# Kernel optimization log

Measured on AMD Instinct MI355X. Metric: run time of the kernel, lower is better.

## Reference

```python
import jax, jax.numpy as jnp
import numpy as np


def setup_inputs() -> dict:
    key = jax.random.key(0)
    k1, k2 = jax.random.split(key)
    node_num = 10000
    n_edges = 640000
    d = 128
    embs = jax.random.normal(k1, (node_num, d), dtype=jnp.float32)
    ratings = jax.random.randint(k2, (n_edges, 2), 0, node_num, dtype=jnp.int32)
    return {"embs": embs, "ratings": ratings, "node_num": node_num}


def reference(embs, ratings, node_num):
    # edge endpoints: row (source) and column (neighbor) indices
    r0 = ratings[:, 0]
    r1 = ratings[:, 1]
    # edge dot-product attention scores  [E]
    scores = jnp.sum(embs[r0] * embs[r1], axis=-1)
    # sparse row-wise softmax (torch.sparse.softmax over dim=1)
    seg_max = jax.ops.segment_max(scores, r0, num_segments=node_num)
    seg_max = jnp.where(jnp.isfinite(seg_max), seg_max, jnp.float32(0.0))  # empty rows
    ex = jnp.exp(scores - seg_max[r0])
    denom = jax.ops.segment_sum(ex, r0, num_segments=node_num)
    attn = ex / denom[r0]
    # attention weights are detached in the original module
    attn = jax.lax.stop_gradient(attn)
    # sparse mm aggregation: out[i] = sum_{e: r0[e]=i} attn[e] * embs[r1[e]]
    out = jax.ops.segment_sum(attn[:, None] * embs[r1], r0, num_segments=node_num)
    return out
```

## Files before the change

### kernel.cpp

```cpp
#include <hip/hip_runtime.h>
#include <hip/hip_bf16.h>
#include <hip/hip_fp16.h>
#include <math.h>


#define K_CHUNKS 256
#define NODE_LDS 10240
#define NPAD 10240
#define STAGE_LDS 2560
#define EXP_CLAMP 80.0f
#define MAXE_N 256

using half2v = _Float16 __attribute__((ext_vector_type(2)));

__device__ __forceinline__ half2v u2h(unsigned int x) {
    return __builtin_bit_cast(half2v, x);
}

__global__ __launch_bounds__(1024) void build_kernel(const int2* __restrict__ ratings,
                             unsigned short* __restrict__ mtmp,
                             unsigned short* __restrict__ staging,
                             const float4* __restrict__ embs4,
                             ushort4* __restrict__ embs16,
                             int n_edges, int node_num, int chunk_size) {
    __shared__ int hist[NODE_LDS];
    __shared__ unsigned short stage[STAGE_LDS];
    __shared__ int lds_ws[16];
    __shared__ int lds_wp[16];

    int tid  = threadIdx.x;
    int lane = tid & 63;
    int wid  = tid >> 6;
    int k    = blockIdx.x;

    for (int i = tid; i < NODE_LDS; i += 1024) hist[i] = 0;
    __syncthreads();

    int base = k * chunk_size;
    int end  = base + chunk_size; if (end > n_edges) end = n_edges;

    int e0i = base + tid, e1i = e0i + 1024, e2i = e1i + 1024;
    bool h0 = e0i < end, h1 = e1i < end, h2 = e2i < end;
    int2 r0v = h0 ? ratings[e0i] : make_int2(0, 0);
    int2 r1v = h1 ? ratings[e1i] : make_int2(0, 0);
    int2 r2v = h2 ? ratings[e2i] : make_int2(0, 0);

    {
        int nf4 = node_num * 32;
        int per = (nf4 + (int)gridDim.x - 1) / (int)gridDim.x;
        int s0 = k * per;
        int s1 = s0 + per; if (s1 > nf4) s1 = nf4;
        for (int i = s0 + tid; i < s1; i += 1024) {
            float4 v = embs4[i];
            __half hx = __float2half(v.x), hy = __float2half(v.y);
            __half hz = __float2half(v.z), hw = __float2half(v.w);
            ushort4 o;
            o.x = *reinterpret_cast<unsigned short*>(&hx);
            o.y = *reinterpret_cast<unsigned short*>(&hy);
            o.z = *reinterpret_cast<unsigned short*>(&hz);
            o.w = *reinterpret_cast<unsigned short*>(&hw);
            embs16[i] = o;
        }
    }

    if (h0) atomicAdd(&hist[r0v.x], 1);
    if (h1) atomicAdd(&hist[r1v.x], 1);
    if (h2) atomicAdd(&hist[r2v.x], 1);
    for (int e = base + 3072 + tid; e < end; e += 1024)
        atomicAdd(&hist[ratings[e].x], 1);
    __syncthreads();

    const int B = NODE_LDS / 1024;
    int b0 = tid * B;
    int c[B];
    int local = 0;
    #pragma unroll
    for (int j = 0; j < B; ++j) {
        c[j] = hist[b0 + j];
        local += c[j];
    }
    int incl = local;
    #pragma unroll
    for (int off = 1; off < 64; off <<= 1) {
        int t = __shfl_up(incl, off, 64);
        if (lane >= off) incl += t;
    }
    if (lane == 63) lds_ws[wid] = incl;
    __syncthreads();
    if (wid == 0 && lane < 16) {
        int wv = lds_ws[lane];
        #pragma unroll
        for (int off = 1; off < 16; off <<= 1) {
            int t = __shfl_up(wv, off, 64);
            if (lane >= off) wv += t;
        }
        lds_wp[lane] = wv;
    }
    __syncthreads();
    int run = ((wid > 0) ? lds_wp[wid - 1] : 0) + (incl - local);

    unsigned int mpack[B / 2];
    #pragma unroll
    for (int j = 0; j < B; ++j) {
        int i = b0 + j;
        int cc = (c[j] > 15) ? 15 : c[j];
        unsigned int m = (((unsigned int)run << 4) | (unsigned int)cc) & 0xffffu;
        if (j & 1) mpack[j >> 1] |= m << 16;
        else       mpack[j >> 1]  = m;
        hist[i] = run;
        run += c[j];
    }
    {
        unsigned int* mrow2 = (unsigned int*)(mtmp + (size_t)k * NPAD) + tid * (B / 2);
        #pragma unroll
        for (int jj = 0; jj < B / 2; ++jj) mrow2[jj] = mpack[jj];
    }
    __syncthreads();

    if (h0) { int p = atomicAdd(&hist[r0v.x], 1); if (p < STAGE_LDS) stage[p] = (unsigned short)r0v.y; }
    if (h1) { int p = atomicAdd(&hist[r1v.x], 1); if (p < STAGE_LDS) stage[p] = (unsigned short)r1v.y; }
    if (h2) { int p = atomicAdd(&hist[r2v.x], 1); if (p < STAGE_LDS) stage[p] = (unsigned short)r2v.y; }
    for (int e = base + 3072 + tid; e < end; e += 1024) {
        int2 r = ratings[e];
        int p = atomicAdd(&hist[r.x], 1);
        if (p < STAGE_LDS) stage[p] = (unsigned short)r.y;
    }
    __syncthreads();

    int nsh = end - base;
    unsigned int* g  = (unsigned int*)(staging + (size_t)k * chunk_size);
    unsigned int* sg = (unsigned int*)stage;
    int nu = (nsh + 1) >> 1;
    for (int i = tid; i < nu; i += 1024) g[i] = sg[i];
}

__global__ __launch_bounds__(256, 8) void node_kernel(
                            const unsigned short* __restrict__ embs16,
                            const unsigned short* __restrict__ mtmp,
                            const unsigned short* __restrict__ staging,
                            float* __restrict__ out,
                            int node_num, int chunk_size) {
    __shared__ int s_r1[4][MAXE_N];

    int tid   = threadIdx.x;
    int lane  = tid & 63;
    int wid   = tid >> 6;
    int g     = lane >> 4;
    int t     = lane & 15;
    int n     = blockIdx.x * 4 + wid;
    bool nvalid = (n < node_num);
    int nc    = nvalid ? n : 0;

    uint4 au = ((const uint4*)(embs16 + (size_t)nc * 128))[t];

    unsigned int f[4];
    #pragma unroll
    for (int j = 0; j < 4; ++j)
        f[j] = mtmp[(size_t)(4 * lane + j) * NPAD + nc];
    int c[4], o[4];
    #pragma unroll
    for (int j = 0; j < 4; ++j) {
        c[j] = nvalid ? (int)(f[j] & 15u) : 0;
        o[j] = (int)(f[j] >> 4);
    }
    int cnt = (c[0] + c[1]) + (c[2] + c[3]);
    int incl = cnt;
    #pragma unroll
    for (int off = 1; off < 64; off <<= 1) {
        int tt = __shfl_up(incl, off, 64);
        if (lane >= off) incl += tt;
    }
    int basep = incl - cnt;
    int E = __shfl(incl, 63, 64);
    if (E > MAXE_N) E = MAXE_N;

    {
        int idx = basep;
        #pragma unroll
        for (int j = 0; j < 4; ++j) {
            if (c[j] > 0) {
                const unsigned short* sp =
                    staging + (size_t)(4 * lane + j) * chunk_size + o[j];
                for (int q = 0; q < c[j]; ++q) {
                    if (idx < MAXE_N) s_r1[wid][idx] = (int)sp[q];
                    ++idx;
                }
            }
        }
    }

    float l = 0.f;
    float acc[8];
    #pragma unroll
    for (int j = 0; j < 8; ++j) acc[j] = 0.f;

    int r1c[4];
    #pragma unroll
    for (int b = 0; b < 4; ++b) {
        int ix = b * 4 + g;
        r1c[b] = (ix < E) ? s_r1[wid][ix] : 0;
    }

    for (int base = 0; base < E; base += 16) {
        uint4 uc[4];
        #pragma unroll
        for (int b = 0; b < 4; ++b)
            uc[b] = ((const uint4*)(embs16 + (size_t)r1c[b] * 128))[t];

        int r1n[4];
        #pragma unroll
        for (int b = 0; b < 4; ++b) {
            int ix = base + 16 + b * 4 + g;
            r1n[b] = (ix < E) ? s_r1[wid][ix] : 0;
        }

        float s[4];
        #pragma unroll
        for (int b = 0; b < 4; ++b) {
            float d = __builtin_amdgcn_fdot2(u2h(uc[b].x), u2h(au.x), 0.f, false);
            d = __builtin_amdgcn_fdot2(u2h(uc[b].y), u2h(au.y), d, false);
            d = __builtin_amdgcn_fdot2(u2h(uc[b].z), u2h(au.z), d, false);
            d = __builtin_amdgcn_fdot2(u2h(uc[b].w), u2h(au.w), d, false);
            s[b] = d;
        }
        #pragma unroll
        for (int b = 0; b < 4; ++b) {
            #pragma unroll
            for (int off = 1; off < 16; off <<= 1)
                s[b] += __shfl_xor(s[b], off, 64);
        }
        float p[4];
        #pragma unroll
        for (int b = 0; b < 4; ++b)
            p[b] = ((base + b * 4 + g) < E) ? __expf(fminf(s[b], EXP_CLAMP)) : 0.f;
        l += (p[0] + p[1]) + (p[2] + p[3]);

        #pragma unroll
        for (int b = 0; b < 4; ++b) {
            half2v h0 = u2h(uc[b].x), h1 = u2h(uc[b].y);
            half2v h2 = u2h(uc[b].z), h3 = u2h(uc[b].w);
            acc[0] = fmaf(p[b], (float)h0[0], acc[0]);
            acc[1] = fmaf(p[b], (float)h0[1], acc[1]);
            acc[2] = fmaf(p[b], (float)h1[0], acc[2]);
            acc[3] = fmaf(p[b], (float)h1[1], acc[3]);
            acc[4] = fmaf(p[b], (float)h2[0], acc[4]);
            acc[5] = fmaf(p[b], (float)h2[1], acc[5]);
            acc[6] = fmaf(p[b], (float)h3[0], acc[6]);
            acc[7] = fmaf(p[b], (float)h3[1], acc[7]);
        }

        #pragma unroll
        for (int b = 0; b < 4; ++b) r1c[b] = r1n[b];
    }

    #pragma unroll
    for (int off = 16; off <= 32; off <<= 1) {
        l += __shfl_xor(l, off, 64);
        #pragma unroll
        for (int j = 0; j < 8; ++j) acc[j] += __shfl_xor(acc[j], off, 64);
    }

    if (g == 0 && nvalid) {
        float inv = (l > 0.f) ? 1.f / l : 0.f;
        float4* orow = (float4*)(out + (size_t)n * 128);
        orow[2 * t]     = make_float4(acc[0] * inv, acc[1] * inv, acc[2] * inv, acc[3] * inv);
        orow[2 * t + 1] = make_float4(acc[4] * inv, acc[5] * inv, acc[6] * inv, acc[7] * inv);
    }
}

extern "C" void kernel_launch(void* const* d_in, const int* in_sizes, int n_in,
                              void* d_out, int out_size, void* d_ws, size_t ws_size,
                              hipStream_t stream) {
    const float* embs    = (const float*)d_in[0];
    const int*   ratings = (const int*)d_in[1];
    const int d        = 128;
    const int node_num = in_sizes[0] / d;
    const int n_edges  = in_sizes[1] / 2;
    float* out = (float*)d_out;

    int chunk_size = (n_edges + K_CHUNKS - 1) / K_CHUNKS;
    if (chunk_size & 1) chunk_size += 1;

    auto align256 = [](size_t x) { return (x + 255) & ~(size_t)255; };
    char* ws = (char*)d_ws;
    unsigned short* mtmp = (unsigned short*)ws;
    ws += align256((size_t)K_CHUNKS * NPAD * 2);
    unsigned short* staging = (unsigned short*)ws;
    ws += align256((size_t)K_CHUNKS * chunk_size * 2 + 32);
    unsigned short* embs16 = (unsigned short*)ws;
    ws += align256((size_t)node_num * 128 * 2);

    build_kernel<<<K_CHUNKS, 1024, 0, stream>>>(
        (const int2*)ratings, mtmp, staging,
        (const float4*)embs, (ushort4*)embs16, n_edges, node_num, chunk_size);

    {
        int blocks = (node_num + 3) / 4;
        node_kernel<<<blocks, 256, 0, stream>>>(
            embs16, mtmp, staging, out, node_num, chunk_size);
    }
}
```

Before: 114.8 us.

## Replace per-chunk LDS bucketing with global-atomic CSR build and pipelined gathers

Replaces the single chunked build kernel, which kept per-chunk histograms and packed 4-bit counts, with a global pipeline: zero counters, a global-atomic histogram fused with the fp16 conversion, a single-block scan, and an atomic scatter into a true CSR. The node kernel then reads row_ptr and copies neighbours directly, removing the 256-way per-chunk lookup and its prefix scan, and it now prefetches the next batch's embedding rows instead of only their indices. This trades one kernel for five launches and moves the edge atomics from LDS to global memory, where they contend more. The per-node edge cap rises to 512.

```diff
diff --git a/kernel.cpp b/kernel.cpp
--- a/kernel.cpp
+++ b/kernel.cpp
@@ -4,12 +4,9 @@
 #include <math.h>
 
 
-#define K_CHUNKS 256
-#define NODE_LDS 10240
-#define NPAD 10240
-#define STAGE_LDS 2560
+#define NODE_PAD 10240
+#define MAXE_N 512
 #define EXP_CLAMP 80.0f
-#define MAXE_N 256
 
 using half2v = _Float16 __attribute__((ext_vector_type(2)));
 
@@ -17,129 +14,92 @@
     return __builtin_bit_cast(half2v, x);
 }
 
-__global__ __launch_bounds__(1024) void build_kernel(const int2* __restrict__ ratings,
-                             unsigned short* __restrict__ mtmp,
-                             unsigned short* __restrict__ staging,
-                             const float4* __restrict__ embs4,
-                             ushort4* __restrict__ embs16,
-                             int n_edges, int node_num, int chunk_size) {
-    __shared__ int hist[NODE_LDS];
-    __shared__ unsigned short stage[STAGE_LDS];
-    __shared__ int lds_ws[16];
-    __shared__ int lds_wp[16];
-
+__global__ __launch_bounds__(1024) void zero_kernel(unsigned int* __restrict__ gcount) {
+    gcount[blockIdx.x * 1024 + threadIdx.x] = 0u;
+}
+
+__global__ __launch_bounds__(256) void hist_conv_kernel(
+        const int2* __restrict__ ratings, unsigned int* __restrict__ gcount,
+        const float4* __restrict__ embs4, ushort4* __restrict__ embs16,
+        int n_edges, int nf4) {
+    int gid    = blockIdx.x * 256 + threadIdx.x;
+    int stride = gridDim.x * 256;
+    for (int e = gid; e < n_edges; e += stride)
+        atomicAdd(&gcount[ratings[e].x], 1u);
+    for (int i = gid; i < nf4; i += stride) {
+        float4 v = embs4[i];
+        __half hx = __float2half(v.x), hy = __float2half(v.y);
+        __half hz = __float2half(v.z), hw = __float2half(v.w);
+        ushort4 o;
+        o.x = *reinterpret_cast<unsigned short*>(&hx);
+        o.y = *reinterpret_cast<unsigned short*>(&hy);
+        o.z = *reinterpret_cast<unsigned short*>(&hz);
+        o.w = *reinterpret_cast<unsigned short*>(&hw);
+        embs16[i] = o;
+    }
+}
+
+__global__ __launch_bounds__(1024) void scan_kernel(
+        const unsigned int* __restrict__ gcount,
+        unsigned int* __restrict__ row_ptr,
+        unsigned int* __restrict__ cursor) {
+    __shared__ unsigned int lds_ws[16];
+    __shared__ unsigned int lds_wp[16];
     int tid  = threadIdx.x;
     int lane = tid & 63;
     int wid  = tid >> 6;
-    int k    = blockIdx.x;
-
-    for (int i = tid; i < NODE_LDS; i += 1024) hist[i] = 0;
-    __syncthreads();
-
-    int base = k * chunk_size;
-    int end  = base + chunk_size; if (end > n_edges) end = n_edges;
-
-    int e0i = base + tid, e1i = e0i + 1024, e2i = e1i + 1024;
-    bool h0 = e0i < end, h1 = e1i < end, h2 = e2i < end;
-    int2 r0v = h0 ? ratings[e0i] : make_int2(0, 0);
-    int2 r1v = h1 ? ratings[e1i] : make_int2(0, 0);
-    int2 r2v = h2 ? ratings[e2i] : make_int2(0, 0);
-
-    {
-        int nf4 = node_num * 32;
-        int per = (nf4 + (int)gridDim.x - 1) / (int)gridDim.x;
-        int s0 = k * per;
-        int s1 = s0 + per; if (s1 > nf4) s1 = nf4;
-        for (int i = s0 + tid; i < s1; i += 1024) {
-            float4 v = embs4[i];
-            __half hx = __float2half(v.x), hy = __float2half(v.y);
-            __half hz = __float2half(v.z), hw = __float2half(v.w);
-            ushort4 o;
-            o.x = *reinterpret_cast<unsigned short*>(&hx);
-            o.y = *reinterpret_cast<unsigned short*>(&hy);
-            o.z = *reinterpret_cast<unsigned short*>(&hz);
-            o.w = *reinterpret_cast<unsigned short*>(&hw);
-            embs16[i] = o;
-        }
-    }
-
-    if (h0) atomicAdd(&hist[r0v.x], 1);
-    if (h1) atomicAdd(&hist[r1v.x], 1);
-    if (h2) atomicAdd(&hist[r2v.x], 1);
-    for (int e = base + 3072 + tid; e < end; e += 1024)
-        atomicAdd(&hist[ratings[e].x], 1);
-    __syncthreads();
-
-    const int B = NODE_LDS / 1024;
+    const int B = NODE_PAD / 1024;
     int b0 = tid * B;
-    int c[B];
-    int local = 0;
-    #pragma unroll
-    for (int j = 0; j < B; ++j) {
-        c[j] = hist[b0 + j];
-        local += c[j];
-    }
-    int incl = local;
+    unsigned int c[B];
+    unsigned int local = 0;
+    #pragma unroll
+    for (int j = 0; j < B; ++j) { c[j] = gcount[b0 + j]; local += c[j]; }
+    unsigned int incl = local;
     #pragma unroll
     for (int off = 1; off < 64; off <<= 1) {
-        int t = __shfl_up(incl, off, 64);
+        unsigned int t = __shfl_up(incl, off, 64);
         if (lane >= off) incl += t;
     }
     if (lane == 63) lds_ws[wid] = incl;
     __syncthreads();
     if (wid == 0 && lane < 16) {
-        int wv = lds_ws[lane];
+        unsigned int wv = lds_ws[lane];
         #pragma unroll
         for (int off = 1; off < 16; off <<= 1) {
-            int t = __shfl_up(wv, off, 64);
+            unsigned int t = __shfl_up(wv, off, 64);
             if (lane >= off) wv += t;
         }
         lds_wp[lane] = wv;
     }
     __syncthreads();
-    int run = ((wid > 0) ? lds_wp[wid - 1] : 0) + (incl - local);
-
-    unsigned int mpack[B / 2];
+    unsigned int run = ((wid > 0) ? lds_wp[wid - 1] : 0) + (incl - local);
     #pragma unroll
     for (int j = 0; j < B; ++j) {
-        int i = b0 + j;
-        int cc = (c[j] > 15) ? 15 : c[j];
-        unsigned int m = (((unsigned int)run << 4) | (unsigned int)cc) & 0xffffu;
-        if (j & 1) mpack[j >> 1] |= m << 16;
-        else       mpack[j >> 1]  = m;
-        hist[i] = run;
+        row_ptr[b0 + j] = run;
+        cursor[b0 + j]  = run;
         run += c[j];
     }
-    {
-        unsigned int* mrow2 = (unsigned int*)(mtmp + (size_t)k * NPAD) + tid * (B / 2);
-        #pragma unroll
-        for (int jj = 0; jj < B / 2; ++jj) mrow2[jj] = mpack[jj];
-    }
-    __syncthreads();
-
-    if (h0) { int p = atomicAdd(&hist[r0v.x], 1); if (p < STAGE_LDS) stage[p] = (unsigned short)r0v.y; }
-    if (h1) { int p = atomicAdd(&hist[r1v.x], 1); if (p < STAGE_LDS) stage[p] = (unsigned short)r1v.y; }
-    if (h2) { int p = atomicAdd(&hist[r2v.x], 1); if (p < STAGE_LDS) stage[p] = (unsigned short)r2v.y; }
-    for (int e = base + 3072 + tid; e < end; e += 1024) {
+    if (tid == 1023) row_ptr[NODE_PAD] = run;
+}
+
+__global__ __launch_bounds__(256) void scatter_kernel(
+        const int2* __restrict__ ratings, unsigned int* __restrict__ cursor,
+        unsigned short* __restrict__ csr, int n_edges) {
+    int gid    = blockIdx.x * 256 + threadIdx.x;
+    int stride = gridDim.x * 256;
+    for (int e = gid; e < n_edges; e += stride) {
         int2 r = ratings[e];
-        int p = atomicAdd(&hist[r.x], 1);
-        if (p < STAGE_LDS) stage[p] = (unsigned short)r.y;
-    }
-    __syncthreads();
-
-    int nsh = end - base;
-    unsigned int* g  = (unsigned int*)(staging + (size_t)k * chunk_size);
-    unsigned int* sg = (unsigned int*)stage;
-    int nu = (nsh + 1) >> 1;
-    for (int i = tid; i < nu; i += 1024) g[i] = sg[i];
-}
-
-__global__ __launch_bounds__(256, 8) void node_kernel(
+        unsigned int p = atomicAdd(&cursor[r.x], 1u);
+        csr[p] = (unsigned short)r.y;
+    }
+}
+
+__global__ __launch_bounds__(256) void node_kernel(
                             const unsigned short* __restrict__ embs16,
-                            const unsigned short* __restrict__ mtmp,
-                            const unsigned short* __restrict__ staging,
+                            const unsigned int* __restrict__ row_ptr,
+                            const unsigned short* __restrict__ csr,
                             float* __restrict__ out,
-                            int node_num, int chunk_size) {
+                            int node_num) {
     __shared__ int s_r1[4][MAXE_N];
 
     int tid   = threadIdx.x;
@@ -151,67 +111,38 @@
     bool nvalid = (n < node_num);
     int nc    = nvalid ? n : 0;
 
+    unsigned int rp0 = row_ptr[nc];
+    unsigned int rp1 = row_ptr[nc + 1];
     uint4 au = ((const uint4*)(embs16 + (size_t)nc * 128))[t];
 
-    unsigned int f[4];
-    #pragma unroll
-    for (int j = 0; j < 4; ++j)
-        f[j] = mtmp[(size_t)(4 * lane + j) * NPAD + nc];
-    int c[4], o[4];
-    #pragma unroll
-    for (int j = 0; j < 4; ++j) {
-        c[j] = nvalid ? (int)(f[j] & 15u) : 0;
-        o[j] = (int)(f[j] >> 4);
-    }
-    int cnt = (c[0] + c[1]) + (c[2] + c[3]);
-    int incl = cnt;
-    #pragma unroll
-    for (int off = 1; off < 64; off <<= 1) {
-        int tt = __shfl_up(incl, off, 64);
-        if (lane >= off) incl += tt;
-    }
-    int basep = incl - cnt;
-    int E = __shfl(incl, 63, 64);
+    int E = nvalid ? (int)(rp1 - rp0) : 0;
     if (E > MAXE_N) E = MAXE_N;
 
-    {
-        int idx = basep;
-        #pragma unroll
-        for (int j = 0; j < 4; ++j) {
-            if (c[j] > 0) {
-                const unsigned short* sp =
-                    staging + (size_t)(4 * lane + j) * chunk_size + o[j];
-                for (int q = 0; q < c[j]; ++q) {
-                    if (idx < MAXE_N) s_r1[wid][idx] = (int)sp[q];
-                    ++idx;
-                }
-            }
-        }
-    }
+    for (int i = lane; i < E; i += 64)
+        s_r1[wid][i] = (int)csr[rp0 + i];
 
     float l = 0.f;
     float acc[8];
     #pragma unroll
     for (int j = 0; j < 8; ++j) acc[j] = 0.f;
 
-    int r1c[4];
+    bool vc[4]; uint4 uc[4];
     #pragma unroll
     for (int b = 0; b < 4; ++b) {
         int ix = b * 4 + g;
-        r1c[b] = (ix < E) ? s_r1[wid][ix] : 0;
+        vc[b] = ix < E;
+        int r1 = vc[b] ? s_r1[wid][ix] : 0;
+        uc[b] = ((const uint4*)(embs16 + (size_t)r1 * 128))[t];
     }
 
     for (int base = 0; base < E; base += 16) {
-        uint4 uc[4];
-        #pragma unroll
-        for (int b = 0; b < 4; ++b)
-            uc[b] = ((const uint4*)(embs16 + (size_t)r1c[b] * 128))[t];
-
-        int r1n[4];
+        bool vn[4]; uint4 un[4];
         #pragma unroll
         for (int b = 0; b < 4; ++b) {
             int ix = base + 16 + b * 4 + g;
-            r1n[b] = (ix < E) ? s_r1[wid][ix] : 0;
+            vn[b] = ix < E;
+            int r1 = vn[b] ? s_r1[wid][ix] : 0;
+            un[b] = ((const uint4*)(embs16 + (size_t)r1 * 128))[t];
         }
 
         float s[4];
@@ -232,7 +163,7 @@
         float p[4];
         #pragma unroll
         for (int b = 0; b < 4; ++b)
-            p[b] = ((base + b * 4 + g) < E) ? __expf(fminf(s[b], EXP_CLAMP)) : 0.f;
+            p[b] = vc[b] ? __expf(fminf(s[b], EXP_CLAMP)) : 0.f;
         l += (p[0] + p[1]) + (p[2] + p[3]);
 
         #pragma unroll
@@ -250,7 +181,7 @@
         }
 
         #pragma unroll
-        for (int b = 0; b < 4; ++b) r1c[b] = r1n[b];
+        for (int b = 0; b < 4; ++b) { uc[b] = un[b]; vc[b] = vn[b]; }
     }
 
     #pragma unroll
@@ -278,25 +209,33 @@
     const int n_edges  = in_sizes[1] / 2;
     float* out = (float*)d_out;
 
-    int chunk_size = (n_edges + K_CHUNKS - 1) / K_CHUNKS;
-    if (chunk_size & 1) chunk_size += 1;
-
     auto align256 = [](size_t x) { return (x + 255) & ~(size_t)255; };
     char* ws = (char*)d_ws;
-    unsigned short* mtmp = (unsigned short*)ws;
-    ws += align256((size_t)K_CHUNKS * NPAD * 2);
-    unsigned short* staging = (unsigned short*)ws;
-    ws += align256((size_t)K_CHUNKS * chunk_size * 2 + 32);
+    unsigned int* gcount = (unsigned int*)ws;
+    ws += align256((size_t)NODE_PAD * 4);
+    unsigned int* row_ptr = (unsigned int*)ws;
+    ws += align256((size_t)(NODE_PAD + 1) * 4);
+    unsigned int* cursor = (unsigned int*)ws;
+    ws += align256((size_t)NODE_PAD * 4);
+    unsigned short* csr = (unsigned short*)ws;
+    ws += align256((size_t)n_edges * 2 + 32);
     unsigned short* embs16 = (unsigned short*)ws;
     ws += align256((size_t)node_num * 128 * 2);
 
-    build_kernel<<<K_CHUNKS, 1024, 0, stream>>>(
-        (const int2*)ratings, mtmp, staging,
-        (const float4*)embs, (ushort4*)embs16, n_edges, node_num, chunk_size);
+    zero_kernel<<<NODE_PAD / 1024, 1024, 0, stream>>>(gcount);
+
+    hist_conv_kernel<<<2048, 256, 0, stream>>>(
+        (const int2*)ratings, gcount,
+        (const float4*)embs, (ushort4*)embs16, n_edges, node_num * 32);
+
+    scan_kernel<<<1, 1024, 0, stream>>>(gcount, row_ptr, cursor);
+
+    scatter_kernel<<<2048, 256, 0, stream>>>(
+        (const int2*)ratings, cursor, csr, n_edges);
 
     {
         int blocks = (node_num + 3) / 4;
         node_kernel<<<blocks, 256, 0, stream>>>(
-            embs16, mtmp, staging, out, node_num, chunk_size);
-    }
-}
+            embs16, row_ptr, csr, out, node_num);
+    }
+}
```

Result: slower. 165.7 us (+44.4%).
